# Kernel optimization log

Measured on AMD Instinct MI355X. Metric: run time of the kernel, lower is better.

The kernel has to match this reference:

```python
import jax, jax.numpy as jnp
import numpy as np

B, C, F, H, W = 2, 512, 8, 32, 32


def setup_inputs() -> dict:
    key = jax.random.key(0)
    ks = jax.random.split(key, 10)
    s = 0.02
    return {
        "x": jax.random.normal(ks[0], (B, C, F, H, W), jnp.float32),
        "gamma": jnp.ones((C, 1, 1, 1), jnp.float32),
        "wq": jax.random.normal(ks[1], (C, C), jnp.float32) * s,
        "bq": jnp.zeros((C,), jnp.float32),
        "wk": jax.random.normal(ks[2], (C, C), jnp.float32) * s,
        "bk": jnp.zeros((C,), jnp.float32),
        "wv": jax.random.normal(ks[3], (C, C), jnp.float32) * s,
        "bv": jnp.zeros((C,), jnp.float32),
        "wo": jax.random.normal(ks[4], (C, C), jnp.float32) * s,
        "bo": jnp.zeros((C,), jnp.float32),
    }


def _rms_norm(x, gamma):
    # F.normalize(x, dim=1) * sqrt(C) * gamma  (channel-first, eps=1e-12)
    n = jnp.sqrt(jnp.sum(x * x, axis=1, keepdims=True))
    return x / jnp.maximum(n, 1e-12) * (x.shape[1] ** 0.5) * gamma


def _conv1x1(x, w, b):
    # 1x1x1 Conv3d == per-voxel linear over channels
    return jnp.einsum("oi,bifhw->bofhw", w, x) + b[None, :, None, None, None]


def reference(x, gamma, wq, bq, wk, bk, wv, bv, wo, bo):
    b, c, f, h, w = x.shape
    n_hw = h * w
    S = f * n_hw

    hn = _rms_norm(x, gamma)
    q = _conv1x1(hn, wq, bq).reshape(b, c, S).swapaxes(1, 2)  # [b, S, c]
    k = _conv1x1(hn, wk, bk).reshape(b, c, S).swapaxes(1, 2)
    v = _conv1x1(hn, wv, bv).reshape(b, c, S).swapaxes(1, 2)

    # block-causal mask: query attends to all tokens in frames <= its own frame
    frame_id = jnp.arange(S) // n_hw
    allow = frame_id[:, None] >= frame_id[None, :]  # [S, S] bool

    scores = jnp.einsum("bsc,btc->bst", q, k) / jnp.sqrt(jnp.asarray(c, x.dtype))
    scores = jnp.where(allow[None], scores, -jnp.inf)
    p = jax.nn.softmax(scores, axis=-1)
    o = jnp.einsum("bst,btc->bsc", p, v)  # [b, S, c]

    o = o.swapaxes(1, 2).reshape(b, c, f, h, w)
    return x + _conv1x1(o, wo, bo)
```

## Files before the change

### kernel.cpp

```cpp
#include <hip/hip_runtime.h>
#include <hip/hip_bf16.h>
#include <math.h>

typedef __bf16 bf16;
typedef __bf16 bf16x8 __attribute__((ext_vector_type(8)));
typedef float f32x4 __attribute__((ext_vector_type(4)));

#define C_DIM 512
#define S_DIM 8192

__device__ __forceinline__ void async_ld16(const void* g, void* l) {
    __builtin_amdgcn_global_load_lds(
        (const __attribute__((address_space(1))) unsigned int*)g,
        (__attribute__((address_space(3))) unsigned int*)l, 16, 0, 0);
}

__device__ __forceinline__ unsigned char to_fp8(float v) {
    return (unsigned char)(__builtin_amdgcn_cvt_pk_fp8_f32(v, v, 0, false) & 0xFF);
}

__global__ void detect_kernel(const unsigned short* __restrict__ xu, int* __restrict__ flag) {
    int j = threadIdx.x;
    for (int i = 16 + j; i < 320; i += 64) flag[i] = 0;
    unsigned e = (xu[2 * j] >> 7) & 0xFF;
    unsigned long long m = __ballot(e >= 90 && e <= 140);
    if (j == 0) *flag = (__popcll(m) >= 48) ? 1 : 0;
}

__global__ __launch_bounds__(256) void convert_kernel(const void* __restrict__ s0,
                                                      const void* __restrict__ s1,
                                                      const void* __restrict__ s2,
                                                      const void* __restrict__ s3,
                                                      bf16* __restrict__ dst,
                                                      const int* __restrict__ flag) {
    int y = blockIdx.y;
    const void* srcs[4] = {s0, s1, s2, s3};
    const void* src = srcs[y];
    int i = blockIdx.x * 256 + threadIdx.x;
    bf16* d = dst + (size_t)y * 262144;
    if (*flag) {
        volatile const bf16* s = (volatile const bf16*)src;
        d[i] = s[i];
    } else {
        volatile const float* s = (volatile const float*)src;
        d[i] = (bf16)s[i];
    }
}

__global__ __launch_bounds__(256) void rms_kernel(const void* __restrict__ x,
                                                  float* __restrict__ r,
                                                  const int* __restrict__ flag) {
    __shared__ float red[4][64];
    int b  = blockIdx.x >> 7;
    int s0 = (blockIdx.x & 127) * 64;
    int sl = threadIdx.x & 63;
    int cq = threadIdx.x >> 6;
    float acc = 0.f;
    if (*flag) {
        const bf16* xp = (const bf16*)x + ((size_t)b * C_DIM + cq * 128) * S_DIM + s0 + sl;
        for (int c = 0; c < 128; ++c) { float v = (float)xp[(size_t)c * S_DIM]; acc += v * v; }
    } else {
        const float* xp = (const float*)x + ((size_t)b * C_DIM + cq * 128) * S_DIM + s0 + sl;
        for (int c = 0; c < 128; ++c) { float v = xp[(size_t)c * S_DIM]; acc += v * v; }
    }
    red[cq][sl] = acc;
    __syncthreads();
    if (cq == 0) {
        float t = red[0][sl] + red[1][sl] + red[2][sl] + red[3][sl];
        r[b * S_DIM + s0 + sl] = 22.627416997969522f / fmaxf(sqrtf(t), 1e-12f);
    }
}

__global__ __launch_bounds__(256) void hn_kernel(const void* __restrict__ x,
                                                 const void* __restrict__ gamma,
                                                 const float* __restrict__ r,
                                                 bf16* __restrict__ hn,
                                                 const int* __restrict__ flag) {
    __shared__ float tile[64][65];
    int f  = *flag;
    int b  = blockIdx.z;
    int c0 = blockIdx.y * 64;
    int s0 = blockIdx.x * 64;
    int col = threadIdx.x & 63;
    int row = threadIdx.x >> 6;
    if (f) {
        const bf16* xp = (const bf16*)x + ((size_t)b * C_DIM + c0) * S_DIM + s0;
        for (int i = 0; i < 16; ++i)
            tile[row + i * 4][col] = (float)xp[(size_t)(row + i * 4) * S_DIM + col];
    } else {
        const float* xp = (const float*)x + ((size_t)b * C_DIM + c0) * S_DIM + s0;
        for (int i = 0; i < 16; ++i)
            tile[row + i * 4][col] = xp[(size_t)(row + i * 4) * S_DIM + col];
    }
    __syncthreads();
    float g;
    if (f) g = (float)((const bf16*)gamma)[c0 + col];
    else   g = ((const float*)gamma)[c0 + col];
    bf16* hp = hn + ((size_t)b * S_DIM + s0) * C_DIM + c0;
    for (int i = 0; i < 16; ++i) {
        int s_l = row + i * 4;
        float rv = r[b * S_DIM + s0 + s_l];
        hp[(size_t)s_l * C_DIM + col] = (bf16)(tile[col][s_l] * rv * g);
    }
}

__global__ __launch_bounds__(256, 2) void gemm_qkv_kernel(const bf16* __restrict__ A,
                                                          const bf16* __restrict__ Wq,
                                                          const bf16* __restrict__ Wk,
                                                          const bf16* __restrict__ Wv,
                                                          const void* __restrict__ bq,
                                                          const void* __restrict__ bk,
                                                          const void* __restrict__ bv,
                                                          unsigned char* __restrict__ oq,
                                                          unsigned char* __restrict__ ok,
                                                          unsigned char* __restrict__ ov,
                                                          const int* __restrict__ flag) {
    __shared__ bf16 As[128 * 40];
    __shared__ bf16 Bqs[128 * 40];
    __shared__ bf16 Bks[128 * 40];
    __shared__ bf16 Bvs[128 * 40];
    int f  = *flag;
    int m0 = blockIdx.x * 128;
    int n0 = blockIdx.y * 128;
    int tid  = threadIdx.x;
    int lane = tid & 63;
    int wave = tid >> 6;
    int wm = (wave & 1) * 64;
    int wn = (wave >> 1) * 64;
    int l15  = lane & 15;
    int quad = lane >> 4;

    f32x4 aq[4][4] = {}, ak[4][4] = {}, av[4][4] = {};
    for (int k0 = 0; k0 < C_DIM; k0 += 32) {
        __syncthreads();
        for (int u = tid; u < 512; u += 256) {
            int rr = u >> 2;
            int cc = (u & 3) * 8;
            *(bf16x8*)&As[rr * 40 + cc]  = *(const bf16x8*)&A [(size_t)(m0 + rr) * C_DIM + k0 + cc];
            *(bf16x8*)&Bqs[rr * 40 + cc] = *(const bf16x8*)&Wq[(size_t)(n0 + rr) * C_DIM + k0 + cc];
            *(bf16x8*)&Bks[rr * 40 + cc] = *(const bf16x8*)&Wk[(size_t)(n0 + rr) * C_DIM + k0 + cc];
            *(bf16x8*)&Bvs[rr * 40 + cc] = *(const bf16x8*)&Wv[(size_t)(n0 + rr) * C_DIM + k0 + cc];
        }
        __syncthreads();
        bf16x8 af[4];
#pragma unroll
        for (int i = 0; i < 4; ++i)
            af[i] = *(bf16x8*)&As[(wm + i * 16 + l15) * 40 + quad * 8];
#pragma unroll
        for (int j = 0; j < 4; ++j) {
            int boff = (wn + j * 16 + l15) * 40 + quad * 8;
            bf16x8 b0 = *(bf16x8*)&Bqs[boff];
#pragma unroll
            for (int i = 0; i < 4; ++i)
                aq[i][j] = __builtin_amdgcn_mfma_f32_16x16x32_bf16(af[i], b0, aq[i][j], 0, 0, 0);
            bf16x8 b1 = *(bf16x8*)&Bks[boff];
#pragma unroll
            for (int i = 0; i < 4; ++i)
                ak[i][j] = __builtin_amdgcn_mfma_f32_16x16x32_bf16(af[i], b1, ak[i][j], 0, 0, 0);
            bf16x8 b2 = *(bf16x8*)&Bvs[boff];
#pragma unroll
            for (int i = 0; i < 4; ++i)
                av[i][j] = __builtin_amdgcn_mfma_f32_16x16x32_bf16(af[i], b2, av[i][j], 0, 0, 0);
        }
    }
#pragma unroll
    for (int i = 0; i < 4; ++i)
#pragma unroll
        for (int j = 0; j < 4; ++j) {
            int n = n0 + wn + j * 16 + l15;
            float bvq = f ? (float)((const bf16*)bq)[n] : ((const float*)bq)[n];
            float bvk = f ? (float)((const bf16*)bk)[n] : ((const float*)bk)[n];
            float bvv = f ? (float)((const bf16*)bv)[n] : ((const float*)bv)[n];
#pragma unroll
            for (int rg = 0; rg < 4; ++rg) {
                int m = m0 + wm + i * 16 + quad * 4 + rg;
                oq[(size_t)m * C_DIM + n] = to_fp8(aq[i][j][rg] + bvq);
                size_t ik = ((((size_t)(m >> 5) * 64 + (n >> 3)) * 32 + (m & 31)) * 8) + (n & 7);
                ok[ik] = to_fp8(ak[i][j][rg] + bvk);
                size_t iv = ((((size_t)(m >> 5) * 4 + ((m >> 3) & 3)) * 512 + n) * 8) + (m & 7);
                ov[iv] = to_fp8(av[i][j][rg] + bvv);
            }
        }
}

__global__ __launch_bounds__(256, 2) void gemm_kernel(const bf16* __restrict__ A,
                                                      const bf16* __restrict__ W,
                                                      const void* __restrict__ bias,
                                                      const void* __restrict__ resid,
                                                      void* __restrict__ out,
                                                      const int* __restrict__ flag) {
    __shared__ bf16 As[128 * 40];
    __shared__ bf16 Bs[128 * 40];
    int f  = *flag;
    int m0 = blockIdx.x * 128;
    int n0 = blockIdx.y * 128;
    int tid  = threadIdx.x;
    int lane = tid & 63;
    int wave = tid >> 6;
    int wm = (wave & 1) * 64;
    int wn = (wave >> 1) * 64;
    int l15  = lane & 15;
    int quad = lane >> 4;

    f32x4 acc[4][4] = {};
    for (int k0 = 0; k0 < C_DIM; k0 += 32) {
        __syncthreads();
        for (int u = tid; u < 512; u += 256) {
            int rrow = u >> 2;
            int cc = (u & 3) * 8;
            *(bf16x8*)&As[rrow * 40 + cc] =
                *(const bf16x8*)&A[(size_t)(m0 + rrow) * C_DIM + k0 + cc];
            *(bf16x8*)&Bs[rrow * 40 + cc] =
                *(const bf16x8*)&W[(size_t)(n0 + rrow) * C_DIM + k0 + cc];
        }
        __syncthreads();
        bf16x8 af[4], bfr[4];
#pragma unroll
        for (int i = 0; i < 4; ++i)
            af[i] = *(bf16x8*)&As[(wm + i * 16 + l15) * 40 + quad * 8];
#pragma unroll
        for (int j = 0; j < 4; ++j)
            bfr[j] = *(bf16x8*)&Bs[(wn + j * 16 + l15) * 40 + quad * 8];
#pragma unroll
        for (int i = 0; i < 4; ++i)
#pragma unroll
            for (int j = 0; j < 4; ++j)
                acc[i][j] = __builtin_amdgcn_mfma_f32_16x16x32_bf16(af[i], bfr[j], acc[i][j], 0, 0, 0);
    }
    if (f) {
        bf16* op = (bf16*)out;
        const bf16* rp = (const bf16*)resid;
#pragma unroll
        for (int i = 0; i < 4; ++i)
#pragma unroll
            for (int j = 0; j < 4; ++j)
#pragma unroll
                for (int rg = 0; rg < 4; ++rg) {
                    int m = m0 + wm + i * 16 + quad * 4 + rg;
                    int n = n0 + wn + j * 16 + l15;
                    float bv = (float)((const bf16*)bias)[n];
                    int b = m >> 13, s = m & 8191;
                    size_t idx = ((size_t)b * C_DIM + n) * S_DIM + s;
                    op[idx] = (bf16)(acc[i][j][rg] + bv + (float)rp[idx]);
                }
    } else {
        float* op = (float*)out;
        const float* rp = (const float*)resid;
#pragma unroll
        for (int i = 0; i < 4; ++i)
#pragma unroll
            for (int j = 0; j < 4; ++j)
#pragma unroll
                for (int rg = 0; rg < 4; ++rg) {
                    int m = m0 + wm + i * 16 + quad * 4 + rg;
                    int n = n0 + wn + j * 16 + l15;
                    float bv = ((const float*)bias)[n];
                    int b = m >> 13, s = m & 8191;
                    size_t idx = ((size_t)b * C_DIM + n) * S_DIM + s;
                    op[idx] = acc[i][j][rg] + bv + rp[idx];
                }
    }
}

__global__ __launch_bounds__(256, 2) void attn_split_kernel(const unsigned char* __restrict__ q,
                                                            const unsigned char* __restrict__ k,
                                                            const unsigned char* __restrict__ vt,
                                                            bf16* __restrict__ part,
                                                            float* __restrict__ lsum,
                                                            int* __restrict__ counter,
                                                            int* __restrict__ cnt,
                                                            int* __restrict__ slist) {
    __shared__ unsigned char Ks[2][16384];
    __shared__ unsigned char Vs[2][16384];
    __shared__ unsigned char Ps[4][16 * 40];
    __shared__ int slot_sh;
    int tid  = threadIdx.x;
    int lane = tid & 63;
    int wave = tid >> 6;
    int l15  = lane & 15;
    int quad = lane >> 4;

    int g0 = blockIdx.x * 72;
    int b_ = (g0 >= 18432) ? 1 : 0;
    int r  = g0 - b_ * 18432;
    int f_ = 0;
    while (r >= 256 * (f_ + 1) * (f_ + 2)) ++f_;
    int L   = 32 * (f_ + 1);
    int rr  = r - 256 * f_ * (f_ + 1);
    int tif = rr / L;
    int cw  = rr - tif * L;

    long qf[16];
    {
        int qbase = (f_ * 16 + tif) * 64 + wave * 16;
        const unsigned char* qp = q + (size_t)(b_ * S_DIM + qbase + l15) * C_DIM;
#pragma unroll
        for (int ks = 0; ks < 16; ++ks)
            qf[ks] = *(const long*)&qp[ks * 32 + quad * 8];
    }

    f32x4 oacc[32] = {};
    float l_i[4] = {0.f, 0.f, 0.f, 0.f};
    const float scale = 0.044194173824159216f;

    {
        const unsigned char* ka = k  + ((size_t)(b_ * 256 + cw) << 14);
        const unsigned char* va = vt + ((size_t)(b_ * 256 + cw) << 14);
#pragma unroll
        for (int j = 0; j < 4; ++j) {
            int base = (j * 4 + wave) * 1024;
            async_ld16(ka + base + lane * 16, &Ks[0][base]);
            async_ld16(va + base + lane * 16, &Vs[0][base]);
        }
    }
    __syncthreads();

    for (int i = 0; i < 72; ++i) {
        int last = (i == 71);
        int nb = b_, nf = f_, nL = L, ntif = tif, ncw = cw + 1;
        int newtile = 0;
        if (ncw == L) {
            ncw = 0; newtile = 1; ntif = tif + 1;
            if (ntif == 16) {
                ntif = 0; nf = f_ + 1; nL = L + 32;
                if (nf == 8) { nf = 0; nL = 32; nb = b_ + 1; }
            }
        }
        if (last) { nb = b_; nf = f_; nL = L; ntif = tif; ncw = cw; newtile = 0; }

        {
            const unsigned char* ka = k  + ((size_t)(nb * 256 + ncw) << 14);
            const unsigned char* va = vt + ((size_t)(nb * 256 + ncw) << 14);
            unsigned char* kd = Ks[(i + 1) & 1];
            unsigned char* vd = Vs[(i + 1) & 1];
#pragma unroll
            for (int j = 0; j < 4; ++j) {
                int base = (j * 4 + wave) * 1024;
                async_ld16(ka + base + lane * 16, kd + base);
                async_ld16(va + base + lane * 16, vd + base);
            }
        }
        const unsigned char* kb = Ks[i & 1];
        const unsigned char* vb = Vs[i & 1];
        f32x4 st[2] = {};
#pragma unroll
        for (int nt = 0; nt < 2; ++nt) {
#pragma unroll
            for (int ks = 0; ks < 16; ++ks) {
                long kf = *(const long*)&kb[(ks * 4 + quad) * 256 + (nt * 16 + l15) * 8];
                st[nt] = __builtin_amdgcn_mfma_f32_16x16x32_fp8_fp8(qf[ks], kf, st[nt], 0, 0, 0);
            }
        }
        float p0[4], p1[4];
#pragma unroll
        for (int rg = 0; rg < 4; ++rg) {
            p0[rg] = __expf(st[0][rg] * scale);
            p1[rg] = __expf(st[1][rg] * scale);
            l_i[rg] += p0[rg] + p1[rg];
        }
        unsigned char* pw = Ps[wave];
#pragma unroll
        for (int rg = 0; rg < 4; ++rg) {
            pw[(quad * 4 + rg) * 40 + l15] = to_fp8(p0[rg]);
            pw[(quad * 4 + rg) * 40 + 16 + l15] = to_fp8(p1[rg]);
        }
        long pf = *(const long*)&pw[l15 * 40 + quad * 8];
#pragma unroll
        for (int dn = 0; dn < 32; ++dn) {
            long vf = *(const long*)&vb[quad * 4096 + (dn * 16 + l15) * 8];
            oacc[dn] = __builtin_amdgcn_mfma_f32_16x16x32_fp8_fp8(pf, vf, oacc[dn], 0, 0, 0);
        }

        if (last || newtile) {
            int ord = b_ * 128 + f_ * 16 + tif;
            if (tid == 0) {
                int s = atomicAdd(counter, 1);
                int pos = atomicAdd(&cnt[ord], 1);
                slist[ord * 8 + pos] = s;
                slot_sh = s;
            }
            __syncthreads();
            int slot = slot_sh;
#pragma unroll
            for (int rg = 0; rg < 4; ++rg)
                for (int d = 1; d < 16; d <<= 1)
                    l_i[rg] += __shfl_xor(l_i[rg], d);
            float rinv[4];
#pragma unroll
            for (int rg = 0; rg < 4; ++rg) rinv[rg] = 1.f / l_i[rg];
            bf16* pp = part + ((size_t)slot * 64 + wave * 16) * C_DIM;
#pragma unroll
            for (int dn = 0; dn < 32; ++dn)
#pragma unroll
                for (int rg = 0; rg < 4; ++rg)
                    pp[(size_t)(quad * 4 + rg) * C_DIM + dn * 16 + l15] =
                        (bf16)(oacc[dn][rg] * rinv[rg]);
            if (l15 == 0) {
#pragma unroll
                for (int rg = 0; rg < 4; ++rg)
                    lsum[slot * 64 + wave * 16 + quad * 4 + rg] = l_i[rg];
            }
            if (!last) {
#pragma unroll
                for (int dn = 0; dn < 32; ++dn) oacc[dn] = (f32x4){0.f, 0.f, 0.f, 0.f};
#pragma unroll
                for (int rg = 0; rg < 4; ++rg) l_i[rg] = 0.f;
                int nqbase = (nf * 16 + ntif) * 64 + wave * 16;
                const unsigned char* qp = q + (size_t)(nb * S_DIM + nqbase + l15) * C_DIM;
#pragma unroll
                for (int ks = 0; ks < 16; ++ks)
                    qf[ks] = *(const long*)&qp[ks * 32 + quad * 8];
            }
        }
        b_ = nb; f_ = nf; L = nL; tif = ntif; cw = ncw;
        __syncthreads();
    }
}

__global__ __launch_bounds__(256, 2) void attn_kernel(const unsigned char* __restrict__ q,
                                                      const unsigned char* __restrict__ k,
                                                      const unsigned char* __restrict__ vt,
                                                      bf16* __restrict__ ob) {
    __shared__ unsigned char Ks[2][16384];
    __shared__ unsigned char Vs[2][16384];
    __shared__ unsigned char Ps[4][16 * 40];
    int id = blockIdx.x;
    int b = id >> 7;
    int t = id & 127;
    int q0 = t * 64;
    int kc1 = ((t >> 4) + 1) << 10;
    int tid  = threadIdx.x;
    int lane = tid & 63;
    int wave = tid >> 6;
    int l15  = lane & 15;
    int quad = lane >> 4;
    int qbase = q0 + wave * 16;
    int nchunks = kc1 >> 5;

    long qf[16];
    const unsigned char* qp = q + (size_t)(b * S_DIM + qbase + l15) * C_DIM;
#pragma unroll
    for (int ks = 0; ks < 16; ++ks)
        qf[ks] = *(const long*)&qp[ks * 32 + quad * 8];

    f32x4 oacc[32] = {};
    float l_i[4] = {0.f, 0.f, 0.f, 0.f};
    const float scale = 0.044194173824159216f;

    const unsigned char* kbase = k  + ((size_t)(b * 256) << 14);
    const unsigned char* vbase = vt + ((size_t)(b * 256) << 14);

#pragma unroll
    for (int j = 0; j < 4; ++j) {
        int base = (j * 4 + wave) * 1024;
        async_ld16(kbase + base + lane * 16, &Ks[0][base]);
        async_ld16(vbase + base + lane * 16, &Vs[0][base]);
    }
    __syncthreads();

    for (int p = 0; p < nchunks; ++p) {
        int pn = (p + 1 < nchunks) ? (p + 1) : p;
        const unsigned char* ksub = kbase + ((size_t)pn << 14);
        const unsigned char* vsub = vbase + ((size_t)pn << 14);
        unsigned char* kd = Ks[(p + 1) & 1];
        unsigned char* vd = Vs[(p + 1) & 1];
#pragma unroll
        for (int j = 0; j < 4; ++j) {
            int base = (j * 4 + wave) * 1024;
            async_ld16(ksub + base + lane * 16, kd + base);
            async_ld16(vsub + base + lane * 16, vd + base);
        }
        const unsigned char* kb = Ks[p & 1];
        const unsigned char* vb = Vs[p & 1];
        f32x4 st[2] = {};
#pragma unroll
        for (int nt = 0; nt < 2; ++nt) {
#pragma unroll
            for (int ks = 0; ks < 16; ++ks) {
                long kf = *(const long*)&kb[(ks * 4 + quad) * 256 + (nt * 16 + l15) * 8];
                st[nt] = __builtin_amdgcn_mfma_f32_16x16x32_fp8_fp8(qf[ks], kf, st[nt], 0, 0, 0);
            }
        }
        float p0[4], p1[4];
#pragma unroll
        for (int rg = 0; rg < 4; ++rg) {
            p0[rg] = __expf(st[0][rg] * scale);
            p1[rg] = __expf(st[1][rg] * scale);
            l_i[rg] += p0[rg] + p1[rg];
        }
        unsigned char* pw = Ps[wave];
#pragma unroll
        for (int rg = 0; rg < 4; ++rg) {
            pw[(quad * 4 + rg) * 40 + l15] = to_fp8(p0[rg]);
            pw[(quad * 4 + rg) * 40 + 16 + l15] = to_fp8(p1[rg]);
        }
        long pf = *(const long*)&pw[l15 * 40 + quad * 8];
#pragma unroll
        for (int dn = 0; dn < 32; ++dn) {
            long vf = *(const long*)&vb[quad * 4096 + (dn * 16 + l15) * 8];
            oacc[dn] = __builtin_amdgcn_mfma_f32_16x16x32_fp8_fp8(pf, vf, oacc[dn], 0, 0, 0);
        }
        __syncthreads();
    }
#pragma unroll
    for (int rg = 0; rg < 4; ++rg)
        for (int d = 1; d < 16; d <<= 1)
            l_i[rg] += __shfl_xor(l_i[rg], d);
    float rinv[4];
#pragma unroll
    for (int rg = 0; rg < 4; ++rg) rinv[rg] = 1.f / l_i[rg];
    bf16* op = ob + (size_t)(b * S_DIM + qbase) * C_DIM;
#pragma unroll
    for (int dn = 0; dn < 32; ++dn)
#pragma unroll
        for (int rg = 0; rg < 4; ++rg)
            op[(size_t)(quad * 4 + rg) * C_DIM + dn * 16 + l15] =
                (bf16)(oacc[dn][rg] * rinv[rg]);
}

__global__ __launch_bounds__(256) void combine_kernel(const bf16* __restrict__ part,
                                                      const float* __restrict__ lsum,
                                                      bf16* __restrict__ ob,
                                                      const int* __restrict__ cnt,
                                                      const int* __restrict__ slist) {
    int id = blockIdx.x;
    int b  = id >> 7;
    int q0 = (id & 127) * 64;
    int U  = cnt[id];
    int qq = threadIdx.x >> 2;
    int cr = threadIdx.x & 3;
    int sl[8];
    float w[8];
    float D = 0.f;
    for (int u = 0; u < U; ++u) {
        sl[u] = slist[id * 8 + u];
        w[u] = lsum[sl[u] * 64 + qq];
        D += w[u];
    }
    float Dinv = 1.f / D;
    for (int u = 0; u < U; ++u) w[u] *= Dinv;
    bf16* op = ob + (size_t)(b * S_DIM + q0 + qq) * C_DIM + cr * 128;
    for (int ch = 0; ch < 16; ++ch) {
        float acc[8] = {};
        for (int u = 0; u < U; ++u) {
            bf16x8 pv = *(const bf16x8*)&part[((size_t)sl[u] * 64 + qq) * C_DIM + cr * 128 + ch * 8];
#pragma unroll
            for (int j = 0; j < 8; ++j) acc[j] += w[u] * (float)pv[j];
        }
        bf16x8 o8;
#pragma unroll
        for (int j = 0; j < 8; ++j) o8[j] = (bf16)acc[j];
        *(bf16x8*)&op[ch * 8] = o8;
    }
}

extern "C" void kernel_launch(void* const* d_in, const int* in_sizes, int n_in,
                              void* d_out, int out_size, void* d_ws, size_t ws_size,
                              hipStream_t stream) {
    const void* x     = d_in[0];
    const void* gamma = d_in[1];
    const void* wq    = d_in[2];
    const void* bq    = d_in[3];
    const void* wk    = d_in[4];
    const void* bk    = d_in[5];
    const void* wv    = d_in[6];
    const void* bv    = d_in[7];
    const void* wo    = d_in[8];
    const void* bo    = d_in[9];

    char* ws = (char*)d_ws;
    int*   flag    = (int*)ws;
    int*   counter = (int*)(ws + 64);
    int*   cntp    = (int*)(ws + 256);
    int*   slist   = (int*)(ws + 0x12000);
    float* r_buf   = (float*)(ws + 4096);
    bf16* wqb = (bf16*)(ws + 0x20000);
    bf16* wkb = (bf16*)(ws + 0xA0000);
    bf16* wvb = (bf16*)(ws + 0x120000);
    bf16* wob = (bf16*)(ws + 0x1A0000);
    float* lsum_buf = (float*)(ws + 0x240000);
    bf16* hn  = (bf16*)(ws + 0x400000);
    unsigned char* qb  = (unsigned char*)(ws + 0x1400000);
    unsigned char* kb  = (unsigned char*)(ws + 0x1C00000);
    unsigned char* vtb = (unsigned char*)(ws + 0x2400000);
    bf16* ob  = (bf16*)(ws + 0x2C00000);
    bf16* part = (bf16*)(ws + 0x5400000);

    const size_t ws_needed_split = 0x5400000ull + 768ull * 64 * 512 * 2;
    int split = (ws_size >= ws_needed_split) ? 1 : 0;

    hipLaunchKernelGGL(detect_kernel, dim3(1), dim3(64), 0, stream,
                       (const unsigned short*)x, flag);
    hipLaunchKernelGGL(convert_kernel, dim3(1024, 4), dim3(256), 0, stream,
                       wq, wk, wv, wo, wqb, flag);
    hipLaunchKernelGGL(rms_kernel, dim3(256), dim3(256), 0, stream, x, r_buf, flag);
    hipLaunchKernelGGL(hn_kernel, dim3(128, 8, 2), dim3(256), 0, stream, x, gamma, r_buf, hn, flag);
    hipLaunchKernelGGL(gemm_qkv_kernel, dim3(128, 4), dim3(256), 0, stream,
                       hn, wqb, wkb, wvb, bq, bk, bv, qb, kb, vtb, flag);
    if (split) {
        hipLaunchKernelGGL(attn_split_kernel, dim3(512), dim3(256), 0, stream,
                           qb, kb, vtb, part, lsum_buf, counter, cntp, slist);
        hipLaunchKernelGGL(combine_kernel, dim3(256), dim3(256), 0, stream,
                           part, lsum_buf, ob, cntp, slist);
    } else {
        hipLaunchKernelGGL(attn_kernel, dim3(256), dim3(256), 0, stream, qb, kb, vtb, ob);
    }
    hipLaunchKernelGGL(gemm_kernel, dim3(128, 4), dim3(256), 0, stream, ob, wob, bo, x, d_out, flag);
}
```

Before: 382.4 us.

## Use 3-buffer K/V LDS ring in split attention and transpose GEMM epilogue via LDS

The split attention kernel swaps its double-buffered K and V arrays (64KB) for a three-slot ring (48KB), which lets three blocks fit per CU and raises the grid from 512 to 768 blocks of 48 chunks each. The V load is issued after the QK MFMAs behind an extra barrier, so the ring can be reused. Separately, the output GEMM epilogue now stages accumulators through LDS so that residual reads and output writes become contiguous vectorised accesses along the spatial dimension instead of scattered scalar ones. The costs are an extra barrier per iteration, less prefetch slack, more partial results for the combine step, and a larger workspace requirement that may fall back to the non-split path.

```diff
diff --git a/kernel.cpp b/kernel.cpp
--- a/kernel.cpp
+++ b/kernel.cpp
@@ -191,6 +191,7 @@
                                                       const int* __restrict__ flag) {
     __shared__ bf16 As[128 * 40];
     __shared__ bf16 Bs[128 * 40];
+    __shared__ float tbuf[4][16][65];
     int f  = *flag;
     int m0 = blockIdx.x * 128;
     int n0 = blockIdx.y * 128;
@@ -227,42 +228,49 @@
             for (int j = 0; j < 4; ++j)
                 acc[i][j] = __builtin_amdgcn_mfma_f32_16x16x32_bf16(af[i], bfr[j], acc[i][j], 0, 0, 0);
     }
-    if (f) {
-        bf16* op = (bf16*)out;
-        const bf16* rp = (const bf16*)resid;
+    int rrow = lane >> 2;
+    int mseg = (lane & 3) << 4;
+    int m_base = m0 + wm;
+    int bb = m_base >> 13;
+    int sb = (m_base & 8191) + mseg;
+#pragma unroll
+    for (int j = 0; j < 4; ++j) {
 #pragma unroll
         for (int i = 0; i < 4; ++i)
-#pragma unroll
-            for (int j = 0; j < 4; ++j)
-#pragma unroll
-                for (int rg = 0; rg < 4; ++rg) {
-                    int m = m0 + wm + i * 16 + quad * 4 + rg;
-                    int n = n0 + wn + j * 16 + l15;
-                    float bv = (float)((const bf16*)bias)[n];
-                    int b = m >> 13, s = m & 8191;
-                    size_t idx = ((size_t)b * C_DIM + n) * S_DIM + s;
-                    op[idx] = (bf16)(acc[i][j][rg] + bv + (float)rp[idx]);
-                }
-    } else {
-        float* op = (float*)out;
-        const float* rp = (const float*)resid;
-#pragma unroll
-        for (int i = 0; i < 4; ++i)
-#pragma unroll
-            for (int j = 0; j < 4; ++j)
-#pragma unroll
-                for (int rg = 0; rg < 4; ++rg) {
-                    int m = m0 + wm + i * 16 + quad * 4 + rg;
-                    int n = n0 + wn + j * 16 + l15;
-                    float bv = ((const float*)bias)[n];
-                    int b = m >> 13, s = m & 8191;
-                    size_t idx = ((size_t)b * C_DIM + n) * S_DIM + s;
-                    op[idx] = acc[i][j][rg] + bv + rp[idx];
-                }
-    }
-}
-
-__global__ __launch_bounds__(256, 2) void attn_split_kernel(const unsigned char* __restrict__ q,
+            *(f32x4*)&tbuf[wave][l15][i * 16 + quad * 4] = acc[i][j];
+        int n = n0 + wn + j * 16 + rrow;
+        if (f) {
+            float bv = (float)((const bf16*)bias)[n];
+            bf16* opb = (bf16*)out + ((size_t)bb * C_DIM + n) * S_DIM + sb;
+            const bf16* rpb = (const bf16*)resid + ((size_t)bb * C_DIM + n) * S_DIM + sb;
+#pragma unroll
+            for (int t = 0; t < 2; ++t) {
+                bf16x8 rv = *(const bf16x8*)&rpb[t * 8];
+                bf16x8 o8;
+#pragma unroll
+                for (int e = 0; e < 8; ++e)
+                    o8[e] = (bf16)(tbuf[wave][rrow][mseg + t * 8 + e] + bv + (float)rv[e]);
+                *(bf16x8*)&opb[t * 8] = o8;
+            }
+        } else {
+            float bv = ((const float*)bias)[n];
+            float* opf = (float*)out + ((size_t)bb * C_DIM + n) * S_DIM + sb;
+            const float* rpf = (const float*)resid + ((size_t)bb * C_DIM + n) * S_DIM + sb;
+#pragma unroll
+            for (int t = 0; t < 4; ++t) {
+                float4 rv = *(const float4*)&rpf[t * 4];
+                float4 v;
+                v.x = tbuf[wave][rrow][mseg + t * 4 + 0] + bv + rv.x;
+                v.y = tbuf[wave][rrow][mseg + t * 4 + 1] + bv + rv.y;
+                v.z = tbuf[wave][rrow][mseg + t * 4 + 2] + bv + rv.z;
+                v.w = tbuf[wave][rrow][mseg + t * 4 + 3] + bv + rv.w;
+                *(float4*)&opf[t * 4] = v;
+            }
+        }
+    }
+}
+
+__global__ __launch_bounds__(256, 3) void attn_split_kernel(const unsigned char* __restrict__ q,
                                                             const unsigned char* __restrict__ k,
                                                             const unsigned char* __restrict__ vt,
                                                             bf16* __restrict__ part,
@@ -270,8 +278,7 @@
                                                             int* __restrict__ counter,
                                                             int* __restrict__ cnt,
                                                             int* __restrict__ slist) {
-    __shared__ unsigned char Ks[2][16384];
-    __shared__ unsigned char Vs[2][16384];
+    __shared__ unsigned char Ring[3][16384];
     __shared__ unsigned char Ps[4][16 * 40];
     __shared__ int slot_sh;
     int tid  = threadIdx.x;
@@ -280,7 +287,7 @@
     int l15  = lane & 15;
     int quad = lane >> 4;
 
-    int g0 = blockIdx.x * 72;
+    int g0 = blockIdx.x * 48;
     int b_ = (g0 >= 18432) ? 1 : 0;
     int r  = g0 - b_ * 18432;
     int f_ = 0;
@@ -303,20 +310,21 @@
     float l_i[4] = {0.f, 0.f, 0.f, 0.f};
     const float scale = 0.044194173824159216f;
 
-    {
-        const unsigned char* ka = k  + ((size_t)(b_ * 256 + cw) << 14);
-        const unsigned char* va = vt + ((size_t)(b_ * 256 + cw) << 14);
+    auto stage16 = [&](unsigned char* dst, const unsigned char* src) {
 #pragma unroll
         for (int j = 0; j < 4; ++j) {
-            int base = (j * 4 + wave) * 1024;
-            async_ld16(ka + base + lane * 16, &Ks[0][base]);
-            async_ld16(va + base + lane * 16, &Vs[0][base]);
-        }
-    }
+            int off = wave * 4096 + j * 1024;
+            async_ld16(src + off + lane * 16, dst + off);
+        }
+    };
+
+    stage16(Ring[0], k  + ((size_t)(b_ * 256 + cw) << 14));
+    stage16(Ring[1], vt + ((size_t)(b_ * 256 + cw) << 14));
     __syncthreads();
 
-    for (int i = 0; i < 72; ++i) {
-        int last = (i == 71);
+    int kcur = 0, vcur = 1, knext = 2;
+    for (int i = 0; i < 48; ++i) {
+        int last = (i == 47);
         int nb = b_, nf = f_, nL = L, ntif = tif, ncw = cw + 1;
         int newtile = 0;
         if (ncw == L) {
@@ -328,20 +336,9 @@
         }
         if (last) { nb = b_; nf = f_; nL = L; ntif = tif; ncw = cw; newtile = 0; }
 
-        {
-            const unsigned char* ka = k  + ((size_t)(nb * 256 + ncw) << 14);
-            const unsigned char* va = vt + ((size_t)(nb * 256 + ncw) << 14);
-            unsigned char* kd = Ks[(i + 1) & 1];
-            unsigned char* vd = Vs[(i + 1) & 1];
-#pragma unroll
-            for (int j = 0; j < 4; ++j) {
-                int base = (j * 4 + wave) * 1024;
-                async_ld16(ka + base + lane * 16, kd + base);
-                async_ld16(va + base + lane * 16, vd + base);
-            }
-        }
-        const unsigned char* kb = Ks[i & 1];
-        const unsigned char* vb = Vs[i & 1];
+        stage16(Ring[knext], k + ((size_t)(nb * 256 + ncw) << 14));
+
+        const unsigned char* kb = Ring[kcur];
         f32x4 st[2] = {};
 #pragma unroll
         for (int nt = 0; nt < 2; ++nt) {
@@ -351,6 +348,12 @@
                 st[nt] = __builtin_amdgcn_mfma_f32_16x16x32_fp8_fp8(qf[ks], kf, st[nt], 0, 0, 0);
             }
         }
+
+        __syncthreads();
+
+        stage16(Ring[kcur], vt + ((size_t)(nb * 256 + ncw) << 14));
+
+        const unsigned char* vb = Ring[vcur];
         float p0[4], p1[4];
 #pragma unroll
         for (int rg = 0; rg < 4; ++rg) {
@@ -412,6 +415,7 @@
                     qf[ks] = *(const long*)&qp[ks * 32 + quad * 8];
             }
         }
+        int t = knext; knext = vcur; vcur = kcur; kcur = t;
         b_ = nb; f_ = nf; L = nL; tif = ntif; cw = ncw;
         __syncthreads();
     }
@@ -586,7 +590,7 @@
     bf16* ob  = (bf16*)(ws + 0x2C00000);
     bf16* part = (bf16*)(ws + 0x5400000);
 
-    const size_t ws_needed_split = 0x5400000ull + 768ull * 64 * 512 * 2;
+    const size_t ws_needed_split = 0x5400000ull + 1024ull * 64 * 512 * 2;
     int split = (ws_size >= ws_needed_split) ? 1 : 0;
 
     hipLaunchKernelGGL(detect_kernel, dim3(1), dim3(64), 0, stream,
@@ -598,7 +602,7 @@
     hipLaunchKernelGGL(gemm_qkv_kernel, dim3(128, 4), dim3(256), 0, stream,
                        hn, wqb, wkb, wvb, bq, bk, bv, qb, kb, vtb, flag);
     if (split) {
-        hipLaunchKernelGGL(attn_split_kernel, dim3(512), dim3(256), 0, stream,
+        hipLaunchKernelGGL(attn_split_kernel, dim3(768), dim3(256), 0, stream,
                            qb, kb, vtb, part, lsum_buf, counter, cntp, slist);
         hipLaunchKernelGGL(combine_kernel, dim3(256), dim3(256), 0, stream,
                            part, lsum_buf, ob, cntp, slist);
```

New measurement: 454.3 us. +18.8%, slower.
